# Kernel tuning notes

Measured on AMD Instinct MI355X. Metric: run time of the kernel, lower is better.

The kernel has to match this reference:

```python
import jax, jax.numpy as jnp
import numpy as np

B, AT, NBR, FEAT = 4, 384, 24, 128


def setup_inputs() -> dict:
    key = jax.random.key(0)
    k1, k2, k3 = jax.random.split(key, 3)
    edge_embedding = jax.random.normal(k1, (B, AT, NBR, FEAT), dtype=jnp.float32)
    nbr_idx = jax.random.randint(k2, (B, AT, NBR), 0, AT, dtype=jnp.int64)
    # periodic-cell offsets: small integers stored as float, compared exactly with ==
    cell_offset = jax.random.randint(k3, (B, AT, NBR, 3), 0, 3).astype(jnp.float32)
    return {"edge_embedding": edge_embedding, "nbr_idx": nbr_idx, "cell_offset": cell_offset}


def reference(edge_embedding, nbr_idx, cell_offset):
    # edge_embedding: (B, At, Nbr, F); nbr_idx: (B, At, Nbr) int; cell_offset: (B, At, Nbr, 3)
    Bn, At, Nbr, F = edge_embedding.shape

    # j_nbr[b,a,j,k] = nbr_idx[b, nbr_idx[b,a,j], k]  -- neighbors of atom j (j-th nbr of a)
    j_nbr = jax.vmap(lambda n: n[n])(nbr_idx)                      # (B, At, Nbr, Nbr)
    # cell_j[b,a,j,k,:] = cell_offset[b, nbr_idx[b,a,j], k, :]
    cell_j = jax.vmap(lambda c, n: c[n])(cell_offset, nbr_idx)     # (B, At, Nbr, Nbr, 3)

    # k_masked[b,a,j,i] = nbr_idx[b,a,i] with diagonal (i==j) set to -1 (exclude k==j)
    eye = jnp.eye(Nbr, dtype=bool)                                 # (Nbr, Nbr) [j, i]
    k_masked = jnp.where(eye[None, None], -1, nbr_idx[:, :, None, :])  # (B, At, Nbr, Nbr)

    # match over k: j_nbr[b,a,j,k] == k_masked[b,a,j,i]
    idx_eq = j_nbr[:, :, :, None, :] == k_masked[:, :, :, :, None]      # (B,At,Nbr,Nbr_i,Nbr_k)
    # cell check: cell_offset[b,a,i,:] == cell_j[b,a,j,k,:] for all 3 coords
    cell_eq = jnp.all(
        cell_offset[:, :, None, :, None, :] == cell_j[:, :, :, None, :, :],
        axis=-1,
    )                                                              # (B,At,Nbr,Nbr_i,Nbr_k)

    mask = jnp.any(idx_eq & cell_eq, axis=-1)                      # (B, At, Nbr_j, Nbr_i)

    # edge_jk[b,a,j,i,:] = edge_embedding[b,a,i,:] where mask else 0
    edge_jk = jnp.where(mask[..., None], edge_embedding[:, :, None, :, :],
                        jnp.zeros((), dtype=edge_embedding.dtype))
    return edge_jk
```

## Files before the change

### kernel.cpp

```cpp
#include <hip/hip_runtime.h>

#define Bb 4
#define AT 384
#define NBR 24
#define FEAT 128
#define ROWQ (FEAT / 4)
#define TILEQ (NBR * ROWQ)
#define NTILES (Bb * AT * NBR)
#define OUTQ ((unsigned)NTILES * TILEQ)

typedef float vfloat4 __attribute__((ext_vector_type(4)));

__global__ __launch_bounds__(256) void mask_kernel(
    const int*   __restrict__ nbr,
    const float* __restrict__ cell,
    unsigned int* __restrict__ ws)
{
    const int ba = blockIdx.x;
    const int b  = ba / AT;
    const int t  = threadIdx.x;

    __shared__ int   s_nbr[NBR];
    __shared__ float s_cell[NBR][3];
    __shared__ int   s_nbrj[NBR][NBR];
    __shared__ float s_cellj[NBR][NBR][3];
    __shared__ int   s_mask[NBR * NBR];

    if (t < NBR) {
        s_nbr[t]     = nbr[ba * NBR + t];
        s_cell[t][0] = cell[(ba * NBR + t) * 3 + 0];
        s_cell[t][1] = cell[(ba * NBR + t) * 3 + 1];
        s_cell[t][2] = cell[(ba * NBR + t) * 3 + 2];
    }
    __syncthreads();

    for (int q = t; q < NBR * NBR; q += 256) {
        const int j = q / NBR;
        const int k = q % NBR;
        const int base = (b * AT + s_nbr[j]) * NBR + k;
        s_nbrj[j][k]     = nbr[base];
        s_cellj[j][k][0] = cell[base * 3 + 0];
        s_cellj[j][k][1] = cell[base * 3 + 1];
        s_cellj[j][k][2] = cell[base * 3 + 2];
    }
    __syncthreads();

    for (int p = t; p < NBR * NBR; p += 256) {
        const int j = p / NBR;
        const int i = p % NBR;
        int m = 0;
        if (i != j) {
            const int   myidx = s_nbr[i];
            const float c0 = s_cell[i][0];
            const float c1 = s_cell[i][1];
            const float c2 = s_cell[i][2];
            #pragma unroll
            for (int k = 0; k < NBR; ++k) {
                if (s_nbrj[j][k] == myidx &&
                    s_cellj[j][k][0] == c0 &&
                    s_cellj[j][k][1] == c1 &&
                    s_cellj[j][k][2] == c2) { m = 1; }
            }
        }
        s_mask[p] = m;
    }
    __syncthreads();

    if (t < NBR) {
        unsigned int w = 0;
        #pragma unroll
        for (int i = 0; i < NBR; ++i)
            w |= (unsigned int)s_mask[t * NBR + i] << i;
        ws[ba * NBR + t] = w;
    }
}

__global__ __launch_bounds__(256) void store_kernel(
    const vfloat4* __restrict__ edge,
    const unsigned int* __restrict__ ws,
    vfloat4*       __restrict__ out)
{
    const vfloat4 zero = (vfloat4)(0.f);
    const unsigned stride = gridDim.x * 256u;
    unsigned q = blockIdx.x * 256u + threadIdx.x;

    for (; q < OUTQ; q += stride) {
        const unsigned tile   = q / TILEQ;
        const unsigned within = q - tile * TILEQ;
        const unsigned w = __builtin_amdgcn_readfirstlane(ws[tile]);
        vfloat4 v = zero;
        if (w) {
            const unsigned i = within >> 5;
            if ((w >> i) & 1u) {
                const unsigned ba = tile / NBR;
                v = edge[(size_t)ba * TILEQ + within];
            }
        }
        out[q] = v;
    }
}

__global__ __launch_bounds__(256) void mono_kernel(
    const float* __restrict__ edge,
    const int*   __restrict__ nbr,
    const float* __restrict__ cell,
    float*       __restrict__ out)
{
    const int blk = blockIdx.x;
    const int j   = blk % NBR;
    const int ba  = blk / NBR;
    const int b   = ba / AT;

    __shared__ int   s_nbrj[NBR];
    __shared__ float s_cellj[NBR][3];
    __shared__ int   s_mask[NBR];

    const int t = threadIdx.x;
    const int jatom = nbr[ba * NBR + j];

    if (t < NBR) {
        const int base = (b * AT + jatom) * NBR + t;
        s_nbrj[t]     = nbr[base];
        s_cellj[t][0] = cell[base * 3 + 0];
        s_cellj[t][1] = cell[base * 3 + 1];
        s_cellj[t][2] = cell[base * 3 + 2];
    }
    __syncthreads();

    if (t < NBR) {
        int m = 0;
        if (t != j) {
            const int   myidx = nbr[ba * NBR + t];
            const float c0 = cell[(ba * NBR + t) * 3 + 0];
            const float c1 = cell[(ba * NBR + t) * 3 + 1];
            const float c2 = cell[(ba * NBR + t) * 3 + 2];
            #pragma unroll
            for (int k = 0; k < NBR; ++k) {
                if (s_nbrj[k] == myidx &&
                    s_cellj[k][0] == c0 &&
                    s_cellj[k][1] == c1 &&
                    s_cellj[k][2] == c2) { m = 1; }
            }
        }
        s_mask[t] = m;
    }
    __syncthreads();

    const float4* __restrict__ erow = (const float4*)(edge + (size_t)ba * NBR * FEAT);
    float4*       __restrict__ orow = (float4*)(out + (size_t)blk * NBR * FEAT);
    const float4 zero = make_float4(0.f, 0.f, 0.f, 0.f);
    #pragma unroll
    for (int it = 0; it < 3; ++it) {
        const int q = t + it * 256;
        const int i = q >> 5;
        float4 v = zero;
        if (s_mask[i]) v = erow[q];
        orow[q] = v;
    }
}

extern "C" void kernel_launch(void* const* d_in, const int* in_sizes, int n_in,
                              void* d_out, int out_size, void* d_ws, size_t ws_size,
                              hipStream_t stream) {
    const float* edge = (const float*)d_in[0];
    const int*   nbr  = (const int*)d_in[1];
    const float* cell = (const float*)d_in[2];
    float*       out  = (float*)d_out;

    const size_t need = (size_t)NTILES * sizeof(unsigned int);
    if (ws_size >= need) {
        unsigned int* ws = (unsigned int*)d_ws;
        mask_kernel<<<Bb * AT, 256, 0, stream>>>(nbr, cell, ws);
        store_kernel<<<2048, 256, 0, stream>>>((const vfloat4*)edge, ws,
                                               (vfloat4*)out);
    } else {
        mono_kernel<<<NTILES, 256, 0, stream>>>(edge, nbr, cell, out);
    }
}
```

Before: 103.1 us.

## Fuse mask and store into cooperative kernel with zero-fill then sparse scatter

Replaces the two-kernel mask+store pipeline with one cooperative kernel. It first zero-fills the whole output, does a grid-wide sync, then computes per-atom masks in shared memory, compacts the matching (j,i) pairs into a list, and scatters only those edge rows. This removes the workspace round-trip and the per-element mask checks during the store. In exchange it adds a grid barrier, atomics on a shared counter, and scattered writes that follow a full zero pass.

```diff
diff --git a/kernel.cpp b/kernel.cpp
--- a/kernel.cpp
+++ b/kernel.cpp
@@ -1,4 +1,7 @@
 #include <hip/hip_runtime.h>
+#include <hip/hip_cooperative_groups.h>
+
+namespace cg = cooperative_groups;
 
 #define Bb 4
 #define AT 384
@@ -8,95 +11,93 @@
 #define TILEQ (NBR * ROWQ)
 #define NTILES (Bb * AT * NBR)
 #define OUTQ ((unsigned)NTILES * TILEQ)
+#define COOP_BLOCKS 1024
 
 typedef float vfloat4 __attribute__((ext_vector_type(4)));
 
-__global__ __launch_bounds__(256) void mask_kernel(
-    const int*   __restrict__ nbr,
-    const float* __restrict__ cell,
-    unsigned int* __restrict__ ws)
+__global__ __launch_bounds__(256) void fused_kernel(
+    const vfloat4* __restrict__ edge,
+    const int*     __restrict__ nbr,
+    const float*   __restrict__ cell,
+    vfloat4*       __restrict__ out)
 {
-    const int ba = blockIdx.x;
-    const int b  = ba / AT;
-    const int t  = threadIdx.x;
+    const int t = threadIdx.x;
+
+    {
+        const vfloat4 zero = (vfloat4)(0.f);
+        const unsigned stride = gridDim.x * 256u;
+        for (unsigned q = blockIdx.x * 256u + t; q < OUTQ; q += stride)
+            out[q] = zero;
+    }
+
+    cg::this_grid().sync();
 
     __shared__ int   s_nbr[NBR];
     __shared__ float s_cell[NBR][3];
     __shared__ int   s_nbrj[NBR][NBR];
     __shared__ float s_cellj[NBR][NBR][3];
-    __shared__ int   s_mask[NBR * NBR];
+    __shared__ int   s_list[NBR * NBR];
+    __shared__ int   s_cnt;
 
-    if (t < NBR) {
-        s_nbr[t]     = nbr[ba * NBR + t];
-        s_cell[t][0] = cell[(ba * NBR + t) * 3 + 0];
-        s_cell[t][1] = cell[(ba * NBR + t) * 3 + 1];
-        s_cell[t][2] = cell[(ba * NBR + t) * 3 + 2];
-    }
-    __syncthreads();
+    for (int ba = blockIdx.x; ba < Bb * AT; ba += gridDim.x) {
+        const int b = ba / AT;
 
-    for (int q = t; q < NBR * NBR; q += 256) {
-        const int j = q / NBR;
-        const int k = q % NBR;
-        const int base = (b * AT + s_nbr[j]) * NBR + k;
-        s_nbrj[j][k]     = nbr[base];
-        s_cellj[j][k][0] = cell[base * 3 + 0];
-        s_cellj[j][k][1] = cell[base * 3 + 1];
-        s_cellj[j][k][2] = cell[base * 3 + 2];
-    }
-    __syncthreads();
+        if (t == 0) s_cnt = 0;
+        if (t < NBR) {
+            s_nbr[t]     = nbr[ba * NBR + t];
+            s_cell[t][0] = cell[(ba * NBR + t) * 3 + 0];
+            s_cell[t][1] = cell[(ba * NBR + t) * 3 + 1];
+            s_cell[t][2] = cell[(ba * NBR + t) * 3 + 2];
+        }
+        __syncthreads();
 
-    for (int p = t; p < NBR * NBR; p += 256) {
-        const int j = p / NBR;
-        const int i = p % NBR;
-        int m = 0;
-        if (i != j) {
-            const int   myidx = s_nbr[i];
-            const float c0 = s_cell[i][0];
-            const float c1 = s_cell[i][1];
-            const float c2 = s_cell[i][2];
-            #pragma unroll
-            for (int k = 0; k < NBR; ++k) {
-                if (s_nbrj[j][k] == myidx &&
-                    s_cellj[j][k][0] == c0 &&
-                    s_cellj[j][k][1] == c1 &&
-                    s_cellj[j][k][2] == c2) { m = 1; }
+        for (int q = t; q < NBR * NBR; q += 256) {
+            const int j = q / NBR;
+            const int k = q % NBR;
+            const int base = (b * AT + s_nbr[j]) * NBR + k;
+            s_nbrj[j][k]     = nbr[base];
+            s_cellj[j][k][0] = cell[base * 3 + 0];
+            s_cellj[j][k][1] = cell[base * 3 + 1];
+            s_cellj[j][k][2] = cell[base * 3 + 2];
+        }
+        __syncthreads();
+
+        for (int p = t; p < NBR * NBR; p += 256) {
+            const int j = p / NBR;
+            const int i = p % NBR;
+            if (i != j) {
+                const int   myidx = s_nbr[i];
+                const float c0 = s_cell[i][0];
+                const float c1 = s_cell[i][1];
+                const float c2 = s_cell[i][2];
+                int m = 0;
+                #pragma unroll
+                for (int k = 0; k < NBR; ++k) {
+                    if (s_nbrj[j][k] == myidx &&
+                        s_cellj[j][k][0] == c0 &&
+                        s_cellj[j][k][1] == c1 &&
+                        s_cellj[j][k][2] == c2) { m = 1; }
+                }
+                if (m) {
+                    const int slot = atomicAdd(&s_cnt, 1);
+                    s_list[slot] = (j << 5) | i;
+                }
             }
         }
-        s_mask[p] = m;
-    }
-    __syncthreads();
+        __syncthreads();
 
-    if (t < NBR) {
-        unsigned int w = 0;
-        #pragma unroll
-        for (int i = 0; i < NBR; ++i)
-            w |= (unsigned int)s_mask[t * NBR + i] << i;
-        ws[ba * NBR + t] = w;
-    }
-}
-
-__global__ __launch_bounds__(256) void store_kernel(
-    const vfloat4* __restrict__ edge,
-    const unsigned int* __restrict__ ws,
-    vfloat4*       __restrict__ out)
-{
-    const vfloat4 zero = (vfloat4)(0.f);
-    const unsigned stride = gridDim.x * 256u;
-    unsigned q = blockIdx.x * 256u + threadIdx.x;
-
-    for (; q < OUTQ; q += stride) {
-        const unsigned tile   = q / TILEQ;
-        const unsigned within = q - tile * TILEQ;
-        const unsigned w = __builtin_amdgcn_readfirstlane(ws[tile]);
-        vfloat4 v = zero;
-        if (w) {
-            const unsigned i = within >> 5;
-            if ((w >> i) & 1u) {
-                const unsigned ba = tile / NBR;
-                v = edge[(size_t)ba * TILEQ + within];
-            }
+        const int cnt  = s_cnt;
+        const int g    = t >> 5;
+        const int lane = t & 31;
+        const vfloat4* __restrict__ erow = edge + (size_t)ba * TILEQ;
+        for (int p = g; p < cnt; p += 8) {
+            const int ji = s_list[p];
+            const int j  = ji >> 5;
+            const int i  = ji & 31;
+            out[((size_t)(ba * NBR + j) * NBR + i) * ROWQ + lane] =
+                erow[i * ROWQ + lane];
         }
-        out[q] = v;
+        __syncthreads();
     }
 }
 
@@ -162,18 +163,18 @@
 extern "C" void kernel_launch(void* const* d_in, const int* in_sizes, int n_in,
                               void* d_out, int out_size, void* d_ws, size_t ws_size,
                               hipStream_t stream) {
-    const float* edge = (const float*)d_in[0];
-    const int*   nbr  = (const int*)d_in[1];
-    const float* cell = (const float*)d_in[2];
-    float*       out  = (float*)d_out;
+    const vfloat4* edge = (const vfloat4*)d_in[0];
+    const int*     nbr  = (const int*)d_in[1];
+    const float*   cell = (const float*)d_in[2];
+    vfloat4*       out  = (vfloat4*)d_out;
 
-    const size_t need = (size_t)NTILES * sizeof(unsigned int);
-    if (ws_size >= need) {
-        unsigned int* ws = (unsigned int*)d_ws;
-        mask_kernel<<<Bb * AT, 256, 0, stream>>>(nbr, cell, ws);
-        store_kernel<<<2048, 256, 0, stream>>>((const vfloat4*)edge, ws,
-                                               (vfloat4*)out);
-    } else {
-        mono_kernel<<<NTILES, 256, 0, stream>>>(edge, nbr, cell, out);
+    void* args[] = { (void*)&edge, (void*)&nbr, (void*)&cell, (void*)&out };
+    hipError_t err = hipLaunchCooperativeKernel(
+        reinterpret_cast<void*>(fused_kernel),
+        dim3(COOP_BLOCKS), dim3(256), args, 0, stream);
+
+    if (err != hipSuccess) {
+        mono_kernel<<<NTILES, 256, 0, stream>>>(
+            (const float*)edge, nbr, cell, (float*)out);
     }
 }
```

New measurement: 246.6 us. 139% more time.
